# Performance work log

Measured on AMD Instinct MI355X. Metric: run time of the kernel, lower is better.

## Reference

```python
import jax, jax.numpy as jnp
import numpy as np

B, T, V = 64, 2048, 512


def setup_inputs() -> dict:
    key = jax.random.key(0)
    k1, k2 = jax.random.split(key)
    probabilities = jax.random.normal(k1, (B, T, V), dtype=jnp.float32)
    lengths = jax.random.randint(k2, (B,), 0, T).astype(jnp.int64)
    return {"probabilities": probabilities, "lengths": lengths}


def reference(probabilities, lengths):
    # probabilities: [B, T, V], lengths: [B]
    tokens = jnp.argmax(probabilities, axis=-1)            # [B, T]
    b, t = tokens.shape
    pos_t = jnp.arange(t)
    valid = pos_t[None, :] < lengths[:, None]              # mask to x[:y]
    # unique_consecutive: keep first element of each run
    prev = jnp.concatenate([jnp.full((b, 1), -1, tokens.dtype), tokens[:, :-1]], axis=1)
    new_run = tokens != prev
    # drop blanks (index 0)
    keep = valid & new_run & (tokens != 0)                 # [B, T]
    out_lengths = jnp.sum(keep, axis=1)                    # [B]
    # stream-compact kept tokens to the left; pad with 0 (fixed width T)
    dest = jnp.cumsum(keep, axis=1) - 1                    # target column if kept
    dest = jnp.where(keep, dest, t)                        # t -> dropped by mode='drop'
    out = jnp.zeros((b, t), dtype=tokens.dtype)
    out = out.at[jnp.arange(b)[:, None], dest].set(tokens, mode='drop')
    return (out, out_lengths)
```

## Files before the change

kernel.cpp:

```cpp
#include <hip/hip_runtime.h>


#define VDIM 512
#define TDIM 2048

typedef float  vfloat4 __attribute__((ext_vector_type(4)));

__global__ __launch_bounds__(256) void argmax_rows(const float* __restrict__ probs,
                                                   int* __restrict__ tokens,
                                                   int nrows) {
    const int tid = threadIdx.x;
    const int w = tid >> 6;
    const int l = tid & 63;
    const int g = l >> 4;
    const int s = l & 15;
    const int row = blockIdx.x * 16 + w * 4 + g;
    if (row >= nrows) return;

    const vfloat4* p = (const vfloat4*)(probs + (size_t)row * VDIM);

    vfloat4 v[8];
    #pragma unroll
    for (int j = 0; j < 8; j++) {
        v[j] = __builtin_nontemporal_load(&p[j * 16 + s]);
    }

    float bv = v[0].x;
    int bi = s * 4;
    #pragma unroll
    for (int j = 0; j < 8; j++) {
        const int base = j * 64 + s * 4;
        const vfloat4 a = v[j];
        if (j > 0) { if (a.x > bv) { bv = a.x; bi = base; } }
        if (a.y > bv) { bv = a.y; bi = base + 1; }
        if (a.z > bv) { bv = a.z; bi = base + 2; }
        if (a.w > bv) { bv = a.w; bi = base + 3; }
    }

    #pragma unroll
    for (int off = 8; off > 0; off >>= 1) {
        float ov = __shfl_xor(bv, off, 16);
        int   oi = __shfl_xor(bi, off, 16);
        if (ov > bv || (ov == bv && oi < bi)) { bv = ov; bi = oi; }
    }

    if (s == 0) tokens[row] = bi;
}

__global__ __launch_bounds__(256) void ctc_compact(const int* __restrict__ tokens,
                                                   const int* __restrict__ lengths,
                                                   int* __restrict__ out,
                                                   int* __restrict__ out_lengths) {
    const int b = blockIdx.x;
    const int tid = threadIdx.x;
    const int t0 = tid * 8;

    const int* row = tokens + (size_t)b * TDIM;

    int4 lo = ((const int4*)(row + t0))[0];
    int4 hi = ((const int4*)(row + t0))[1];
    int tok[8] = { lo.x, lo.y, lo.z, lo.w, hi.x, hi.y, hi.z, hi.w };
    int prev = (t0 == 0) ? -1 : row[t0 - 1];

    int len = lengths[b];
    if (len < 0) len = 0;
    if (len > TDIM) len = TDIM;

    int pos[8];
    unsigned kb = 0;
    int c = 0;
    #pragma unroll
    for (int j = 0; j < 8; j++) {
        int t = t0 + j;
        int tk = tok[j];
        bool keep = (t < len) & (tk != 0) & (tk != prev);
        pos[j] = c;
        if (keep) { kb |= (1u << j); c++; }
        prev = tk;
    }

    int lane = tid & 63;
    int wid = tid >> 6;
    int incl = c;
    #pragma unroll
    for (int off = 1; off < 64; off <<= 1) {
        int n = __shfl_up(incl, off, 64);
        if (lane >= off) incl += n;
    }
    __shared__ int wsum[4];
    if (lane == 63) wsum[wid] = incl;
    __syncthreads();
    int wbase = 0;
    #pragma unroll
    for (int w = 0; w < 4; w++) {
        int s = wsum[w];
        if (w < wid) wbase += s;
    }
    int excl = wbase + incl - c;
    int total = wsum[0] + wsum[1] + wsum[2] + wsum[3];

    int* orow = out + (size_t)b * TDIM;
    #pragma unroll
    for (int j = 0; j < 8; j++) {
        if ((kb >> j) & 1u) orow[excl + pos[j]] = tok[j];
    }
    for (int t = total + tid; t < TDIM; t += 256) orow[t] = 0;

    if (tid == 0) out_lengths[b] = total;
}

extern "C" void kernel_launch(void* const* d_in, const int* in_sizes, int n_in,
                              void* d_out, int out_size, void* d_ws, size_t ws_size,
                              hipStream_t stream) {
    (void)d_ws; (void)ws_size; (void)n_in; (void)out_size;
    const float* probs = (const float*)d_in[0];
    const int* lengths = (const int*)d_in[1];
    int* out = (int*)d_out;

    const int B = in_sizes[1];
    const int nrows = in_sizes[0] / VDIM;

    int* tokens = out;

    argmax_rows<<<(nrows + 15) / 16, 256, 0, stream>>>(probs, tokens, nrows);
    ctc_compact<<<B, 256, 0, stream>>>(tokens, lengths, out, out + nrows);
}
```

Before: 330.6 us.

## Fuse argmax and CTC compaction into one cooperative persistent kernel

Replaces the two-kernel sequence (argmax per row, then per-batch compaction) with a single cooperative kernel. A fixed grid of 1024 blocks strides over row groups computing argmax, performs a grid-wide sync, then the first B blocks do the scan-and-compact. This removes one kernel launch and its inter-kernel gap, but adds grid-sync overhead and cuts the number of resident blocks that hide memory latency. It also switches the probability loads from nontemporal to ordinary loads.

```diff
diff --git a/kernel.cpp b/kernel.cpp
--- a/kernel.cpp
+++ b/kernel.cpp
@@ -1,61 +1,60 @@
 #include <hip/hip_runtime.h>
+#include <hip/hip_cooperative_groups.h>
 
 
 #define VDIM 512
 #define TDIM 2048
 
-typedef float  vfloat4 __attribute__((ext_vector_type(4)));
+namespace cg = cooperative_groups;
 
-__global__ __launch_bounds__(256) void argmax_rows(const float* __restrict__ probs,
-                                                   int* __restrict__ tokens,
-                                                   int nrows) {
+__global__ __launch_bounds__(256) void ctc_fused(const float* __restrict__ probs,
+                                                 const int* __restrict__ lengths,
+                                                 int* __restrict__ out,
+                                                 int* __restrict__ out_lengths,
+                                                 int nrows, int B) {
     const int tid = threadIdx.x;
     const int w = tid >> 6;
     const int l = tid & 63;
     const int g = l >> 4;
     const int s = l & 15;
-    const int row = blockIdx.x * 16 + w * 4 + g;
-    if (row >= nrows) return;
 
-    const vfloat4* p = (const vfloat4*)(probs + (size_t)row * VDIM);
+    const int ngroups = nrows >> 4;
+    for (int grp = blockIdx.x; grp < ngroups; grp += gridDim.x) {
+        const int row = grp * 16 + w * 4 + g;
 
-    vfloat4 v[8];
-    #pragma unroll
-    for (int j = 0; j < 8; j++) {
-        v[j] = __builtin_nontemporal_load(&p[j * 16 + s]);
+        const float4* p = (const float4*)(probs + (size_t)row * VDIM);
+        float4 v[8];
+        #pragma unroll
+        for (int j = 0; j < 8; j++) v[j] = p[j * 16 + s];
+
+        float bv = v[0].x;
+        int bi = s * 4;
+        #pragma unroll
+        for (int j = 0; j < 8; j++) {
+            const int base = j * 64 + s * 4;
+            const float4 a = v[j];
+            if (j > 0) { if (a.x > bv) { bv = a.x; bi = base; } }
+            if (a.y > bv) { bv = a.y; bi = base + 1; }
+            if (a.z > bv) { bv = a.z; bi = base + 2; }
+            if (a.w > bv) { bv = a.w; bi = base + 3; }
+        }
+
+        #pragma unroll
+        for (int off = 8; off > 0; off >>= 1) {
+            float ov = __shfl_xor(bv, off, 16);
+            int   oi = __shfl_xor(bi, off, 16);
+            if (ov > bv || (ov == bv && oi < bi)) { bv = ov; bi = oi; }
+        }
+
+        if (s == 0) out[row] = bi;
     }
 
-    float bv = v[0].x;
-    int bi = s * 4;
-    #pragma unroll
-    for (int j = 0; j < 8; j++) {
-        const int base = j * 64 + s * 4;
-        const vfloat4 a = v[j];
-        if (j > 0) { if (a.x > bv) { bv = a.x; bi = base; } }
-        if (a.y > bv) { bv = a.y; bi = base + 1; }
-        if (a.z > bv) { bv = a.z; bi = base + 2; }
-        if (a.w > bv) { bv = a.w; bi = base + 3; }
-    }
+    cg::this_grid().sync();
 
-    #pragma unroll
-    for (int off = 8; off > 0; off >>= 1) {
-        float ov = __shfl_xor(bv, off, 16);
-        int   oi = __shfl_xor(bi, off, 16);
-        if (ov > bv || (ov == bv && oi < bi)) { bv = ov; bi = oi; }
-    }
-
-    if (s == 0) tokens[row] = bi;
-}
-
-__global__ __launch_bounds__(256) void ctc_compact(const int* __restrict__ tokens,
-                                                   const int* __restrict__ lengths,
-                                                   int* __restrict__ out,
-                                                   int* __restrict__ out_lengths) {
+    if (blockIdx.x >= B) return;
     const int b = blockIdx.x;
-    const int tid = threadIdx.x;
     const int t0 = tid * 8;
-
-    const int* row = tokens + (size_t)b * TDIM;
+    const int* row = out + (size_t)b * TDIM;
 
     int4 lo = ((const int4*)(row + t0))[0];
     int4 hi = ((const int4*)(row + t0))[1];
@@ -92,9 +91,9 @@
     __syncthreads();
     int wbase = 0;
     #pragma unroll
-    for (int w = 0; w < 4; w++) {
-        int s = wsum[w];
-        if (w < wid) wbase += s;
+    for (int ww = 0; ww < 4; ww++) {
+        int ssum = wsum[ww];
+        if (ww < wid) wbase += ssum;
     }
     int excl = wbase + incl - c;
     int total = wsum[0] + wsum[1] + wsum[2] + wsum[3];
@@ -117,11 +116,12 @@
     const int* lengths = (const int*)d_in[1];
     int* out = (int*)d_out;
 
-    const int B = in_sizes[1];
-    const int nrows = in_sizes[0] / VDIM;
+    int B = in_sizes[1];
+    int nrows = in_sizes[0] / VDIM;
+    int* out_lengths = out + nrows;
 
-    int* tokens = out;
-
-    argmax_rows<<<(nrows + 15) / 16, 256, 0, stream>>>(probs, tokens, nrows);
-    ctc_compact<<<B, 256, 0, stream>>>(tokens, lengths, out, out + nrows);
+    void* args[] = { (void*)&probs, (void*)&lengths, (void*)&out,
+                     (void*)&out_lengths, (void*)&nrows, (void*)&B };
+    hipLaunchCooperativeKernel((void*)ctc_fused, dim3(1024), dim3(256),
+                               args, 0, stream);
 }
```

Result: slower. 464.4 us (+40.5%).
